# Optimization experiments

Hardware: AMD Instinct MI355X
Metric: run time of the kernel (lower is better)

Reference implementation:

```python
import jax, jax.numpy as jnp
import numpy as np

# SSD prior config (small VGGLite-style)
FEATURE_MAPS = [10, 5, 3, 1]
BOXES_PER_LOC = [4, 4, 4, 4]
IMG = 128      # ssd_config.DATA.SHAPE[0] -> WhereTransformer image_size
OBJ = 64
ZWHAT = 64
HID = 512
B = 4
N_OBJ = sum(f * f for f in FEATURE_MAPS)                       # 135
N_FEAT = sum(b * f * f for f, b in zip(FEATURE_MAPS, BOXES_PER_LOC))  # 540


def reconstruction_indices():
    # Replicates Decoder.reconstruction_indices: map per-location latents to per-box slots.
    idx = []
    last = 0
    for f, bpl in zip(FEATURE_MAPS, BOXES_PER_LOC):
        for i in range(f * f):
            idx.extend([last + i] * bpl)
        last += f * f
    return np.asarray(idx, dtype=np.int32)


def what_decode(z, W1, b1, W2, b2):
    # WhatDecoder: MLP z_what -> 3xOBJxOBJ object glyph in (0,1)
    h = jax.nn.relu(z @ W1 + b1)
    return jax.nn.sigmoid(h @ W2 + b2).reshape(-1, 3, OBJ, OBJ)


def where_stn(imgs, zw):
    # WhereTransformer: paste each object image into its (cx, cy, w, h) box on an IMGxIMG canvas
    # via inverse-affine bilinear sampling with zero padding (STN / grid_sample semantics).
    cx, cy, w, h = zw[:, 0], zw[:, 1], zw[:, 2], zw[:, 3]
    w = jnp.maximum(w, 1e-2)
    h = jnp.maximum(h, 1e-2)
    lin = jnp.linspace(-1.0, 1.0, IMG)
    gy, gx = jnp.meshgrid(lin, lin, indexing='ij')           # (IMG, IMG)
    u = (gx[None] - (2.0 * cx - 1.0)[:, None, None]) / w[:, None, None]
    v = (gy[None] - (2.0 * cy - 1.0)[:, None, None]) / h[:, None, None]
    px = (u + 1.0) * 0.5 * (OBJ - 1)                          # (N, IMG, IMG)
    py = (v + 1.0) * 0.5 * (OBJ - 1)

    def sample_one(img, py, px):  # img: (3, OBJ, OBJ)
        x0 = jnp.floor(px); y0 = jnp.floor(py)
        wx = px - x0; wy = py - y0
        x0i = x0.astype(jnp.int32); y0i = y0.astype(jnp.int32)

        def tap(yi, xi, wgt):
            valid = (yi >= 0) & (yi < OBJ) & (xi >= 0) & (xi < OBJ)
            yc = jnp.clip(yi, 0, OBJ - 1)
            xc = jnp.clip(xi, 0, OBJ - 1)
            return img[:, yc, xc] * (wgt * valid)[None]

        return (tap(y0i, x0i, (1 - wy) * (1 - wx)) + tap(y0i, x0i + 1, (1 - wy) * wx)
                + tap(y0i + 1, x0i, wy * (1 - wx)) + tap(y0i + 1, x0i + 1, wy * wx))

    return jax.vmap(sample_one)(imgs, py, px)                 # (N, 3, IMG, IMG)


def setup_inputs() -> dict:
    key = jax.random.key(0)
    ks = jax.random.split(key, 8)
    return {
        'z_what': jax.random.normal(ks[0], (B, N_OBJ, ZWHAT), jnp.float32),
        'z_where': jax.random.uniform(ks[1], (B, N_FEAT, 4), jnp.float32),
        'z_depth': jax.random.normal(ks[2], (B, N_OBJ, 1), jnp.float32),
        'W1': jax.random.normal(ks[3], (ZWHAT, HID), jnp.float32) * 0.05,
        'b1': jnp.zeros((HID,), jnp.float32),
        'W2': jax.random.normal(ks[4], (HID, 3 * OBJ * OBJ), jnp.float32) * 0.02,
        'b2': jnp.zeros((3 * OBJ * OBJ,), jnp.float32),
        'z_present': jax.random.randint(ks[5], (B, N_FEAT, 1), 0, 2, jnp.int32),
    }


def reference(z_what, z_where, z_depth, W1, b1, W2, b2, z_present):
    idx = jnp.asarray(reconstruction_indices())
    # index_select: replicate per-location latents across boxes-per-location
    zw_full = z_what[:, idx]                                  # (B, N_FEAT, ZWHAT)
    zd_full = z_depth[:, idx]                                 # (B, N_FEAT, 1)
    # sort descending by depth; gather all latents in that order
    order = jnp.argsort(-zd_full[..., 0], axis=1)             # (B, N_FEAT)
    s_what = jnp.take_along_axis(zw_full, order[..., None], axis=1)
    s_where = jnp.take_along_axis(z_where, order[..., None], axis=1)
    s_pres = jnp.take_along_axis(z_present, order[..., None], axis=1)
    # decode + STN warp all objects; absent objects are zeroed (equivalent to the
    dec = what_decode(s_what.reshape(-1, ZWHAT), W1, b1, W2, b2)
    warped = where_stn(dec, s_where.reshape(-1, 4))
    imgs = warped.reshape(B, N_FEAT, 3, IMG, IMG) * s_pres.astype(warped.dtype)[..., None, None]
    # depth compositing: per channel-pixel, take the first nonzero value in sorted order
    nz = imgs != 0
    first = jnp.argmax(nz, axis=1)                            # (B, 3, IMG, IMG)
    out = jnp.take_along_axis(imgs, first[:, None], axis=1)[:, 0] * nz.any(axis=1)
    return out
```

## Files before the change

kernel.cpp:

```cpp
#include <hip/hip_runtime.h>
#include <hip/hip_bf16.h>
#include <math.h>

#define NBOX  540
#define NOBJ  135
#define ZW    64
#define HIDN  512
#define NOUT  12288
#define OBJS  64
#define BATCH 4
#define MROWS 540
#define MPAD  640

#define PRE_SORT   4
#define PRE_GEMM1  MPAD
#define PRE_CVT    ((NOUT / 64) * (HIDN / 64))
#define PRE_BLOCKS (PRE_SORT + PRE_GEMM1 + PRE_CVT)

#define OFF_N      0u
#define OFF_PARAMS 256u
#define OFF_OBJS   34816u
#define OFF_HBF    43520u
#define OFF_W2T    698880u
#define OFF_DEC    13281792u

typedef short  bf16x8 __attribute__((ext_vector_type(8)));
typedef float  f32x4  __attribute__((ext_vector_type(4)));

#define GLOAD_LDS16(gp, lp)                                                    \
  __builtin_amdgcn_global_load_lds(                                            \
      (const __attribute__((address_space(1))) void*)(gp),                     \
      (__attribute__((address_space(3))) void*)(lp), 16, 0, 0)

__device__ __forceinline__ unsigned short f2bf(float x) {
  __hip_bfloat16 h = __float2bfloat16(x);
  return *(unsigned short*)&h;
}

__global__ __launch_bounds__(256) void k_pre(
    const float* __restrict__ z_depth,
    const float* __restrict__ z_where,
    const int*   __restrict__ z_present,
    const float* __restrict__ Z,
    const float* __restrict__ W1,
    const float* __restrict__ b1,
    const float* __restrict__ W2,
    float4* __restrict__ params,
    int*    __restrict__ objs,
    int*    __restrict__ n_present,
    unsigned short* __restrict__ Hbf,
    unsigned short* __restrict__ W2T)
{
  __shared__ unsigned long long keys[256];
  __shared__ int wsums[4], woff[4];
  __shared__ float zs[ZW];
  __shared__ unsigned int T[64 * 36];

  const int bid = blockIdx.x;
  const int t   = threadIdx.x;

  if (bid < PRE_SORT) {
    const int b = bid;
    unsigned long long key = ~0ull;
    if (t < NOBJ) {
      unsigned u = __float_as_uint(z_depth[b * NOBJ + t]);
      u = (u & 0x80000000u) ? ~u : (u | 0x80000000u);
      key = ((unsigned long long)(~u) << 32) | (unsigned)t;
    }
    keys[t] = key;
    __syncthreads();
    for (int k = 2; k <= 256; k <<= 1) {
      for (int j = k >> 1; j > 0; j >>= 1) {
        int ixj = t ^ j;
        if (ixj > t) {
          unsigned long long a = keys[t], c = keys[ixj];
          bool asc = (t & k) == 0;
          if (asc ? (a > c) : (a < c)) { keys[t] = c; keys[ixj] = a; }
        }
        __syncthreads();
      }
    }
    int boxq[3]; int presq[3]; int cnt = 0;
#pragma unroll
    for (int q = 0; q < 3; q++) {
      int e = 3 * t + q;
      presq[q] = 0; boxq[q] = 0;
      if (e < NBOX) {
        int o  = (int)(keys[e >> 2] & 0xFFFFFFFFull);
        int bx = o * 4 + (e & 3);
        boxq[q]  = bx;
        presq[q] = (z_present[b * NBOX + bx] != 0) ? 1 : 0;
        cnt += presq[q];
      }
    }
    int lane = t & 63, wv = t >> 6;
    int incl = cnt;
#pragma unroll
    for (int o = 1; o < 64; o <<= 1) {
      int vprev = __shfl_up(incl, o, 64);
      if (lane >= o) incl += vprev;
    }
    if (lane == 63) wsums[wv] = incl;
    __syncthreads();
    if (t == 0) {
      int a = 0;
#pragma unroll
      for (int i = 0; i < 4; i++) { woff[i] = a; a += wsums[i]; }
      n_present[b] = a;
    }
    __syncthreads();
    int slot = woff[wv] + incl - cnt;
#pragma unroll
    for (int q = 0; q < 3; q++) {
      if (presq[q]) {
        const float* zw = z_where + ((size_t)b * NBOX + boxq[q]) * 4;
        params[b * NBOX + slot] = make_float4(zw[0], zw[1], zw[2], zw[3]);
        objs[b * NBOX + slot]   = boxq[q] >> 2;
        slot++;
      }
    }
  } else if (bid < PRE_SORT + PRE_GEMM1) {
    const int r = bid - PRE_SORT;
    if (r >= MROWS) {
      Hbf[(size_t)r * HIDN + t] = 0;
      Hbf[(size_t)r * HIDN + t + 256] = 0;
      return;
    }
    if (t < ZW) zs[t] = Z[(size_t)r * ZW + t];
    __syncthreads();
    float a0 = b1[t], a1 = b1[t + 256];
#pragma unroll 8
    for (int k = 0; k < ZW; k++) {
      float z = zs[k];
      a0 += z * W1[(size_t)k * HIDN + t];
      a1 += z * W1[(size_t)k * HIDN + t + 256];
    }
    Hbf[(size_t)r * HIDN + t]       = f2bf(fmaxf(a0, 0.f));
    Hbf[(size_t)r * HIDN + t + 256] = f2bf(fmaxf(a1, 0.f));
  } else {
    const int c  = bid - PRE_SORT - PRE_GEMM1;
    const int n0 = (c % (NOUT / 64)) * 64;
    const int k0 = (c / (NOUT / 64)) * 64;
#pragma unroll
    for (int p = 0; p < 2; p++) {
      int kp = p * 16 + (t >> 4);
      int n4 = t & 15;
      int k  = k0 + kp * 2;
      float4 a = *(const float4*)&W2[(size_t)k * NOUT + n0 + n4 * 4];
      float4 b = *(const float4*)&W2[(size_t)(k + 1) * NOUT + n0 + n4 * 4];
      T[(n4*4 + 0) * 36 + kp] = (unsigned)f2bf(a.x) | ((unsigned)f2bf(b.x) << 16);
      T[(n4*4 + 1) * 36 + kp] = (unsigned)f2bf(a.y) | ((unsigned)f2bf(b.y) << 16);
      T[(n4*4 + 2) * 36 + kp] = (unsigned)f2bf(a.z) | ((unsigned)f2bf(b.z) << 16);
      T[(n4*4 + 3) * 36 + kp] = (unsigned)f2bf(a.w) | ((unsigned)f2bf(b.w) << 16);
    }
    __syncthreads();
#pragma unroll
    for (int p = 0; p < 2; p++) {
      int cc = p * 256 + t;
      int n = cc >> 3, ch = cc & 7;
      uint4 v = *(const uint4*)&T[n * 36 + ch * 4];
      *(uint4*)&W2T[(size_t)(n0 + n) * HIDN + k0 + ch * 8] = v;
    }
  }
}

__global__ __launch_bounds__(256) void k_gemm2_mfma(
    const unsigned short* __restrict__ Hbf,
    const unsigned short* __restrict__ W2T,
    const float* __restrict__ b2,
    float* __restrict__ dec)
{
  __shared__ unsigned short As[128 * 32];
  __shared__ unsigned short Bs[128 * 32];
  const int t    = threadIdx.x;
  const int lane = t & 63, wv = t >> 6;
  const int n0 = blockIdx.x * 128;
  const int m0 = blockIdx.y * 128;
  const int wm = (wv & 1) * 64, wn = (wv >> 1) * 64;

  const int r0 = t >> 2;
  const int kc0 = (t & 3) ^ (r0 & 3);
  const int r1 = r0 + 64;
  const int kc1 = (t & 3) ^ (r1 & 3);

  const int fr = lane & 15;
  const int fj = lane >> 4;
  f32x4 acc[4][4] = {};

  for (int k0 = 0; k0 < HIDN; k0 += 32) {
    GLOAD_LDS16(Hbf + (size_t)(m0 + r0) * HIDN + k0 + kc0 * 8, &As[t * 8]);
    GLOAD_LDS16(Hbf + (size_t)(m0 + r1) * HIDN + k0 + kc1 * 8, &As[(t + 256) * 8]);
    GLOAD_LDS16(W2T + (size_t)(n0 + r0) * HIDN + k0 + kc0 * 8, &Bs[t * 8]);
    GLOAD_LDS16(W2T + (size_t)(n0 + r1) * HIDN + k0 + kc1 * 8, &Bs[(t + 256) * 8]);
    __syncthreads();

    bf16x8 av[4], bv[4];
#pragma unroll
    for (int mi = 0; mi < 4; mi++) {
      int row = wm + mi * 16 + fr;
      av[mi] = *(const bf16x8*)&As[(row * 4 + (fj ^ (row & 3))) * 8];
    }
#pragma unroll
    for (int ni = 0; ni < 4; ni++) {
      int row = wn + ni * 16 + fr;
      bv[ni] = *(const bf16x8*)&Bs[(row * 4 + (fj ^ (row & 3))) * 8];
    }
#pragma unroll
    for (int mi = 0; mi < 4; mi++)
#pragma unroll
      for (int ni = 0; ni < 4; ni++)
        acc[mi][ni] = __builtin_amdgcn_mfma_f32_16x16x32_bf16(av[mi], bv[ni], acc[mi][ni], 0, 0, 0);
    __syncthreads();
  }

#pragma unroll
  for (int ni = 0; ni < 4; ni++) {
    int col = n0 + wn + ni * 16 + fr;
    float bb = b2[col];
#pragma unroll
    for (int mi = 0; mi < 4; mi++) {
#pragma unroll
      for (int r = 0; r < 4; r++) {
        int row = m0 + wm + mi * 16 + fj * 4 + r;
        if (row < MROWS) {
          float v = acc[mi][ni][r] + bb;
          dec[(size_t)row * NOUT + col] = 1.0f / (1.0f + __expf(-v));
        }
      }
    }
  }
}

__global__ __launch_bounds__(256) void k_composite(
    const float4* __restrict__ params, const int* __restrict__ objs,
    const int* __restrict__ n_present, const float* __restrict__ dec,
    float* __restrict__ out)
{
#pragma clang fp contract(off)
  __shared__ float4 sp[NBOX];
  __shared__ int sobj[NBOX];
  const int bid  = blockIdx.x;
  const int t    = threadIdx.x;
  const int b    = bid >> 6;
  const int tile = bid & 63;
  const int y = (tile >> 3) * 16 + (t >> 4);
  const int x = (tile & 7) * 16 + (t & 15);
  const int n = n_present[b];
  for (int i = t; i < n; i += 256) {
    sp[i]   = params[b * NBOX + i];
    sobj[i] = objs[b * NBOX + i];
  }
  __syncthreads();

  const double step = 2.0 / 127.0;
  const double gx = (x == 127) ? 1.0 : ((double)x * step + (-1.0));
  const double gy = (y == 127) ? 1.0 : ((double)y * step + (-1.0));

  float o0 = 0.f, o1 = 0.f, o2 = 0.f;
  bool done = false;
  for (int j = 0; j < n; j++) {
    if (__all((int)done)) break;
    if (!done) {
      float4 p = sp[j];
      double w = fmax((double)p.z, 0.01);
      double h = fmax((double)p.w, 0.01);
      double tx = 2.0 * (double)p.x - 1.0;
      double ty = 2.0 * (double)p.y - 1.0;
      double u = (gx - tx) / w;
      double v = (gy - ty) / h;
      double px = (u + 1.0) * 0.5 * 63.0;
      double py = (v + 1.0) * 0.5 * 63.0;
      double fx = floor(px), fy = floor(py);
      double wx = px - fx, wy = py - fy;
      int x0 = (int)fx, y0 = (int)fy;
      int x1 = x0 + 1, y1 = y0 + 1;
      bool vx0 = (x0 >= 0) && (x0 < OBJS);
      bool vx1 = (x1 >= 0) && (x1 < OBJS);
      bool vy0 = (y0 >= 0) && (y0 < OBJS);
      bool vy1 = (y1 >= 0) && (y1 < OBJS);
      double w00 = (1.0 - wy) * (1.0 - wx);
      double w01 = (1.0 - wy) * wx;
      double w10 = wy * (1.0 - wx);
      double w11 = wy * wx;
      bool c00 = vy0 && vx0 && (w00 > 0.0);
      bool c01 = vy0 && vx1 && (w01 > 0.0);
      bool c10 = vy1 && vx0 && (w10 > 0.0);
      bool c11 = vy1 && vx1 && (w11 > 0.0);
      if (c00 | c01 | c10 | c11) {
        const float* g = dec + (size_t)(b * NOBJ + sobj[j]) * NOUT;
        double s0 = 0.0, s1 = 0.0, s2 = 0.0;
        if (c00) { int o = y0*64 + x0; s0 += g[o]*w00; s1 += g[4096+o]*w00; s2 += g[8192+o]*w00; }
        if (c01) { int o = y0*64 + x1; s0 += g[o]*w01; s1 += g[4096+o]*w01; s2 += g[8192+o]*w01; }
        if (c10) { int o = y1*64 + x0; s0 += g[o]*w10; s1 += g[4096+o]*w10; s2 += g[8192+o]*w10; }
        if (c11) { int o = y1*64 + x1; s0 += g[o]*w11; s1 += g[4096+o]*w11; s2 += g[8192+o]*w11; }
        o0 = (float)s0; o1 = (float)s1; o2 = (float)s2;
        done = true;
      }
    }
  }
  const int ob = b * 3 * 16384 + y * 128 + x;
  out[ob]         = o0;
  out[ob + 16384] = o1;
  out[ob + 32768] = o2;
}

extern "C" void kernel_launch(void* const* d_in, const int* in_sizes, int n_in,
                              void* d_out, int out_size, void* d_ws, size_t ws_size,
                              hipStream_t stream) {
  (void)in_sizes; (void)n_in; (void)out_size; (void)ws_size;
  const float* z_what    = (const float*)d_in[0];
  const float* z_where   = (const float*)d_in[1];
  const float* z_depth   = (const float*)d_in[2];
  const float* W1        = (const float*)d_in[3];
  const float* b1        = (const float*)d_in[4];
  const float* W2        = (const float*)d_in[5];
  const float* b2        = (const float*)d_in[6];
  const int*   z_present = (const int*)d_in[7];
  float* out = (float*)d_out;
  char* ws = (char*)d_ws;

  int*            n_present = (int*)(ws + OFF_N);
  float4*         params    = (float4*)(ws + OFF_PARAMS);
  int*            objs      = (int*)(ws + OFF_OBJS);
  unsigned short* Hbf       = (unsigned short*)(ws + OFF_HBF);
  unsigned short* W2T       = (unsigned short*)(ws + OFF_W2T);
  float*          dec       = (float*)(ws + OFF_DEC);

  k_pre<<<dim3(PRE_BLOCKS), dim3(256), 0, stream>>>(
      z_depth, z_where, z_present, z_what, W1, b1, W2,
      params, objs, n_present, Hbf, W2T);
  k_gemm2_mfma<<<dim3(NOUT / 128, MPAD / 128), dim3(256), 0, stream>>>(Hbf, W2T, b2, dec);
  k_composite<<<dim3(256), dim3(256), 0, stream>>>(params, objs, n_present, dec, out);
}
```

Measured before the change: 138.5 us.

## Precompute per-pixel winning objects and decode only visible objects in GEMM

After: 151.2 us. 1.09x slower.

```diff
diff --git a/kernel.cpp b/kernel.cpp
--- a/kernel.cpp
+++ b/kernel.cpp
@@ -9,20 +9,20 @@
 #define NOUT  12288
 #define OBJS  64
 #define BATCH 4
-#define MROWS 540
-#define MPAD  640
-
-#define PRE_SORT   4
-#define PRE_GEMM1  MPAD
-#define PRE_CVT    ((NOUT / 64) * (HIDN / 64))
-#define PRE_BLOCKS (PRE_SORT + PRE_GEMM1 + PRE_CVT)
-
-#define OFF_N      0u
-#define OFF_PARAMS 256u
-#define OFF_OBJS   34816u
-#define OFF_HBF    43520u
-#define OFF_W2T    698880u
-#define OFF_DEC    13281792u
+
+#define ROLE_WIN   256
+#define ROLE_G1    540
+#define ROLE_CVT   ((NOUT / 64) * (HIDN / 64))
+#define PRE_BLOCKS (ROLE_WIN + ROLE_G1 + ROLE_CVT)
+
+#define OFF_NROWS  0u
+#define OFF_USED   256u
+#define OFF_REMAP  2560u
+#define OFF_ROWOBJ 4864u
+#define OFF_PXWIN  7680u
+#define OFF_HBF    269824u
+#define OFF_W2T    925184u
+#define OFF_DEC    13508096u
 
 typedef short  bf16x8 __attribute__((ext_vector_type(8)));
 typedef float  f32x4  __attribute__((ext_vector_type(4)));
@@ -45,22 +45,30 @@
     const float* __restrict__ W1,
     const float* __restrict__ b1,
     const float* __restrict__ W2,
-    float4* __restrict__ params,
-    int*    __restrict__ objs,
-    int*    __restrict__ n_present,
+    int* __restrict__ nrowsp,
+    int* __restrict__ used,
+    int* __restrict__ remap,
+    int* __restrict__ rowobj,
+    int* __restrict__ pxwin,
     unsigned short* __restrict__ Hbf,
     unsigned short* __restrict__ W2T)
 {
   __shared__ unsigned long long keys[256];
-  __shared__ int wsums[4], woff[4];
+  __shared__ float4 sw[NBOX];
+  __shared__ unsigned char spres[NBOX];
   __shared__ float zs[ZW];
   __shared__ unsigned int T[64 * 36];
 
   const int bid = blockIdx.x;
   const int t   = threadIdx.x;
 
-  if (bid < PRE_SORT) {
-    const int b = bid;
+  if (bid < ROLE_WIN) {
+#pragma clang fp contract(off)
+    const int b    = bid >> 6;
+    const int tile = bid & 63;
+    const int y = (tile >> 3) * 16 + (t >> 4);
+    const int x = (tile & 7) * 16 + (t & 15);
+
     unsigned long long key = ~0ull;
     if (t < NOBJ) {
       unsigned u = __float_as_uint(z_depth[b * NOBJ + t]);
@@ -68,6 +76,10 @@
       key = ((unsigned long long)(~u) << 32) | (unsigned)t;
     }
     keys[t] = key;
+    for (int i = t; i < NBOX; i += 256) {
+      sw[i]    = ((const float4*)z_where)[b * NBOX + i];
+      spres[i] = (unsigned char)(z_present[b * NBOX + i] != 0);
+    }
     __syncthreads();
     for (int k = 2; k <= 256; k <<= 1) {
       for (int j = k >> 1; j > 0; j >>= 1) {
@@ -80,52 +92,61 @@
         __syncthreads();
       }
     }
-    int boxq[3]; int presq[3]; int cnt = 0;
-#pragma unroll
-    for (int q = 0; q < 3; q++) {
-      int e = 3 * t + q;
-      presq[q] = 0; boxq[q] = 0;
-      if (e < NBOX) {
-        int o  = (int)(keys[e >> 2] & 0xFFFFFFFFull);
-        int bx = o * 4 + (e & 3);
-        boxq[q]  = bx;
-        presq[q] = (z_present[b * NBOX + bx] != 0) ? 1 : 0;
-        cnt += presq[q];
+
+    const double step = 2.0 / 127.0;
+    const double gx = (x == 127) ? 1.0 : ((double)x * step + (-1.0));
+    const double gy = (y == 127) ? 1.0 : ((double)y * step + (-1.0));
+    const int lane = t & 63;
+
+    bool done = false;
+    int  win  = -1;
+    for (int e = 0; e < NBOX; e++) {
+      if (__all((int)done)) break;
+      const int o  = (int)(keys[e >> 2] & 0xFFFFFFFFull);
+      const int bx = o * 4 + (e & 3);
+      if (!spres[bx]) continue;
+      bool newly = false;
+      if (!done) {
+        float4 p = sw[bx];
+        double w = fmax((double)p.z, 0.01);
+        double h = fmax((double)p.w, 0.01);
+        double tx = 2.0 * (double)p.x - 1.0;
+        double ty = 2.0 * (double)p.y - 1.0;
+        double u = (gx - tx) / w;
+        double v = (gy - ty) / h;
+        double px = (u + 1.0) * 0.5 * 63.0;
+        double py = (v + 1.0) * 0.5 * 63.0;
+        double fx = floor(px), fy = floor(py);
+        double wx = px - fx, wy = py - fy;
+        int x0 = (int)fx, y0 = (int)fy;
+        int x1 = x0 + 1, y1 = y0 + 1;
+        bool vx0 = (x0 >= 0) && (x0 < OBJS);
+        bool vx1 = (x1 >= 0) && (x1 < OBJS);
+        bool vy0 = (y0 >= 0) && (y0 < OBJS);
+        bool vy1 = (y1 >= 0) && (y1 < OBJS);
+        double w00 = (1.0 - wy) * (1.0 - wx);
+        double w01 = (1.0 - wy) * wx;
+        double w10 = wy * (1.0 - wx);
+        double w11 = wy * wx;
+        bool c00 = vy0 && vx0 && (w00 > 0.0);
+        bool c01 = vy0 && vx1 && (w01 > 0.0);
+        bool c10 = vy1 && vx0 && (w10 > 0.0);
+        bool c11 = vy1 && vx1 && (w11 > 0.0);
+        if (c00 | c01 | c10 | c11) { win = bx; done = true; newly = true; }
       }
-    }
-    int lane = t & 63, wv = t >> 6;
-    int incl = cnt;
-#pragma unroll
-    for (int o = 1; o < 64; o <<= 1) {
-      int vprev = __shfl_up(incl, o, 64);
-      if (lane >= o) incl += vprev;
-    }
-    if (lane == 63) wsums[wv] = incl;
-    __syncthreads();
-    if (t == 0) {
-      int a = 0;
-#pragma unroll
-      for (int i = 0; i < 4; i++) { woff[i] = a; a += wsums[i]; }
-      n_present[b] = a;
-    }
-    __syncthreads();
-    int slot = woff[wv] + incl - cnt;
-#pragma unroll
-    for (int q = 0; q < 3; q++) {
-      if (presq[q]) {
-        const float* zw = z_where + ((size_t)b * NBOX + boxq[q]) * 4;
-        params[b * NBOX + slot] = make_float4(zw[0], zw[1], zw[2], zw[3]);
-        objs[b * NBOX + slot]   = boxq[q] >> 2;
-        slot++;
+      unsigned long long nm = __ballot((int)newly);
+      if (nm != 0ull && lane == (int)__builtin_ctzll(nm)) {
+        int oi = b * NOBJ + o;
+        if (atomicCAS(&used[oi], 0, 1) == 0) {
+          int rr = atomicAdd(nrowsp, 1);
+          rowobj[rr] = oi;
+          remap[oi]  = rr;
+        }
       }
     }
-  } else if (bid < PRE_SORT + PRE_GEMM1) {
-    const int r = bid - PRE_SORT;
-    if (r >= MROWS) {
-      Hbf[(size_t)r * HIDN + t] = 0;
-      Hbf[(size_t)r * HIDN + t + 256] = 0;
-      return;
-    }
+    pxwin[b * 16384 + y * 128 + x] = win;
+  } else if (bid < ROLE_WIN + ROLE_G1) {
+    const int r = bid - ROLE_WIN;
     if (t < ZW) zs[t] = Z[(size_t)r * ZW + t];
     __syncthreads();
     float a0 = b1[t], a1 = b1[t + 256];
@@ -138,7 +159,7 @@
     Hbf[(size_t)r * HIDN + t]       = f2bf(fmaxf(a0, 0.f));
     Hbf[(size_t)r * HIDN + t + 256] = f2bf(fmaxf(a1, 0.f));
   } else {
-    const int c  = bid - PRE_SORT - PRE_GEMM1;
+    const int c  = bid - ROLE_WIN - ROLE_G1;
     const int n0 = (c % (NOUT / 64)) * 64;
     const int k0 = (c / (NOUT / 64)) * 64;
 #pragma unroll
@@ -168,42 +189,62 @@
     const unsigned short* __restrict__ Hbf,
     const unsigned short* __restrict__ W2T,
     const float* __restrict__ b2,
+    const int* __restrict__ nrowsp,
+    const int* __restrict__ rowobj,
     float* __restrict__ dec)
 {
-  __shared__ unsigned short As[128 * 32];
-  __shared__ unsigned short Bs[128 * 32];
+  __shared__ unsigned short As[2][128 * 32];
+  __shared__ unsigned short Bs[2][128 * 32];
+  const int nr = *nrowsp;
+  int bid = (int)blockIdx.x;
+  bid = (bid & 7) * 60 + (bid >> 3);
+  const int m0 = (bid / 96) * 128;
+  if (m0 >= nr) return;
+  const int n0 = (bid % 96) * 128;
+
   const int t    = threadIdx.x;
   const int lane = t & 63, wv = t >> 6;
-  const int n0 = blockIdx.x * 128;
-  const int m0 = blockIdx.y * 128;
   const int wm = (wv & 1) * 64, wn = (wv >> 1) * 64;
 
-  const int r0 = t >> 2;
+  const int r0  = t >> 2;
   const int kc0 = (t & 3) ^ (r0 & 3);
-  const int r1 = r0 + 64;
+  const int r1  = r0 + 64;
   const int kc1 = (t & 3) ^ (r1 & 3);
+
+  const int ga0 = (m0 + r0 < nr) ? rowobj[m0 + r0] : 0;
+  const int ga1 = (m0 + r1 < nr) ? rowobj[m0 + r1] : 0;
+  const unsigned short* a0p = Hbf + (size_t)ga0 * HIDN + kc0 * 8;
+  const unsigned short* a1p = Hbf + (size_t)ga1 * HIDN + kc1 * 8;
+  const unsigned short* b0p = W2T + (size_t)(n0 + r0) * HIDN + kc0 * 8;
+  const unsigned short* b1p = W2T + (size_t)(n0 + r1) * HIDN + kc1 * 8;
 
   const int fr = lane & 15;
   const int fj = lane >> 4;
   f32x4 acc[4][4] = {};
 
-  for (int k0 = 0; k0 < HIDN; k0 += 32) {
-    GLOAD_LDS16(Hbf + (size_t)(m0 + r0) * HIDN + k0 + kc0 * 8, &As[t * 8]);
-    GLOAD_LDS16(Hbf + (size_t)(m0 + r1) * HIDN + k0 + kc1 * 8, &As[(t + 256) * 8]);
-    GLOAD_LDS16(W2T + (size_t)(n0 + r0) * HIDN + k0 + kc0 * 8, &Bs[t * 8]);
-    GLOAD_LDS16(W2T + (size_t)(n0 + r1) * HIDN + k0 + kc1 * 8, &Bs[(t + 256) * 8]);
-    __syncthreads();
-
+#define STAGE(buf, koff)                                                       \
+  do {                                                                         \
+    GLOAD_LDS16(a0p + (koff), &As[buf][t * 8]);                                \
+    GLOAD_LDS16(a1p + (koff), &As[buf][(t + 256) * 8]);                        \
+    GLOAD_LDS16(b0p + (koff), &Bs[buf][t * 8]);                                \
+    GLOAD_LDS16(b1p + (koff), &Bs[buf][(t + 256) * 8]);                        \
+  } while (0)
+
+  STAGE(0, 0);
+  __syncthreads();
+  int cur = 0;
+  for (int kt = 0; kt < HIDN / 32; ++kt) {
+    if (kt < HIDN / 32 - 1) STAGE(cur ^ 1, (kt + 1) * 32);
     bf16x8 av[4], bv[4];
 #pragma unroll
     for (int mi = 0; mi < 4; mi++) {
       int row = wm + mi * 16 + fr;
-      av[mi] = *(const bf16x8*)&As[(row * 4 + (fj ^ (row & 3))) * 8];
+      av[mi] = *(const bf16x8*)&As[cur][(row * 4 + (fj ^ (row & 3))) * 8];
     }
 #pragma unroll
     for (int ni = 0; ni < 4; ni++) {
       int row = wn + ni * 16 + fr;
-      bv[ni] = *(const bf16x8*)&Bs[(row * 4 + (fj ^ (row & 3))) * 8];
+      bv[ni] = *(const bf16x8*)&Bs[cur][(row * 4 + (fj ^ (row & 3))) * 8];
     }
 #pragma unroll
     for (int mi = 0; mi < 4; mi++)
@@ -211,7 +252,9 @@
       for (int ni = 0; ni < 4; ni++)
         acc[mi][ni] = __builtin_amdgcn_mfma_f32_16x16x32_bf16(av[mi], bv[ni], acc[mi][ni], 0, 0, 0);
     __syncthreads();
+    cur ^= 1;
   }
+#undef STAGE
 
 #pragma unroll
   for (int ni = 0; ni < 4; ni++) {
@@ -222,81 +265,65 @@
 #pragma unroll
       for (int r = 0; r < 4; r++) {
         int row = m0 + wm + mi * 16 + fj * 4 + r;
-        if (row < MROWS) {
-          float v = acc[mi][ni][r] + bb;
-          dec[(size_t)row * NOUT + col] = 1.0f / (1.0f + __expf(-v));
-        }
+        float v = acc[mi][ni][r] + bb;
+        dec[(size_t)row * NOUT + col] = 1.0f / (1.0f + __expf(-v));
       }
     }
   }
 }
 
 __global__ __launch_bounds__(256) void k_composite(
-    const float4* __restrict__ params, const int* __restrict__ objs,
-    const int* __restrict__ n_present, const float* __restrict__ dec,
+    const int* __restrict__ pxwin, const int* __restrict__ remap,
+    const float* __restrict__ z_where, const float* __restrict__ dec,
     float* __restrict__ out)
 {
 #pragma clang fp contract(off)
-  __shared__ float4 sp[NBOX];
-  __shared__ int sobj[NBOX];
   const int bid  = blockIdx.x;
   const int t    = threadIdx.x;
   const int b    = bid >> 6;
   const int tile = bid & 63;
   const int y = (tile >> 3) * 16 + (t >> 4);
   const int x = (tile & 7) * 16 + (t & 15);
-  const int n = n_present[b];
-  for (int i = t; i < n; i += 256) {
-    sp[i]   = params[b * NBOX + i];
-    sobj[i] = objs[b * NBOX + i];
-  }
-  __syncthreads();
-
-  const double step = 2.0 / 127.0;
-  const double gx = (x == 127) ? 1.0 : ((double)x * step + (-1.0));
-  const double gy = (y == 127) ? 1.0 : ((double)y * step + (-1.0));
-
+
+  const int win = pxwin[b * 16384 + y * 128 + x];
   float o0 = 0.f, o1 = 0.f, o2 = 0.f;
-  bool done = false;
-  for (int j = 0; j < n; j++) {
-    if (__all((int)done)) break;
-    if (!done) {
-      float4 p = sp[j];
-      double w = fmax((double)p.z, 0.01);
-      double h = fmax((double)p.w, 0.01);
-      double tx = 2.0 * (double)p.x - 1.0;
-      double ty = 2.0 * (double)p.y - 1.0;
-      double u = (gx - tx) / w;
-      double v = (gy - ty) / h;
-      double px = (u + 1.0) * 0.5 * 63.0;
-      double py = (v + 1.0) * 0.5 * 63.0;
-      double fx = floor(px), fy = floor(py);
-      double wx = px - fx, wy = py - fy;
-      int x0 = (int)fx, y0 = (int)fy;
-      int x1 = x0 + 1, y1 = y0 + 1;
-      bool vx0 = (x0 >= 0) && (x0 < OBJS);
-      bool vx1 = (x1 >= 0) && (x1 < OBJS);
-      bool vy0 = (y0 >= 0) && (y0 < OBJS);
-      bool vy1 = (y1 >= 0) && (y1 < OBJS);
-      double w00 = (1.0 - wy) * (1.0 - wx);
-      double w01 = (1.0 - wy) * wx;
-      double w10 = wy * (1.0 - wx);
-      double w11 = wy * wx;
-      bool c00 = vy0 && vx0 && (w00 > 0.0);
-      bool c01 = vy0 && vx1 && (w01 > 0.0);
-      bool c10 = vy1 && vx0 && (w10 > 0.0);
-      bool c11 = vy1 && vx1 && (w11 > 0.0);
-      if (c00 | c01 | c10 | c11) {
-        const float* g = dec + (size_t)(b * NOBJ + sobj[j]) * NOUT;
-        double s0 = 0.0, s1 = 0.0, s2 = 0.0;
-        if (c00) { int o = y0*64 + x0; s0 += g[o]*w00; s1 += g[4096+o]*w00; s2 += g[8192+o]*w00; }
-        if (c01) { int o = y0*64 + x1; s0 += g[o]*w01; s1 += g[4096+o]*w01; s2 += g[8192+o]*w01; }
-        if (c10) { int o = y1*64 + x0; s0 += g[o]*w10; s1 += g[4096+o]*w10; s2 += g[8192+o]*w10; }
-        if (c11) { int o = y1*64 + x1; s0 += g[o]*w11; s1 += g[4096+o]*w11; s2 += g[8192+o]*w11; }
-        o0 = (float)s0; o1 = (float)s1; o2 = (float)s2;
-        done = true;
-      }
-    }
+  if (win >= 0) {
+    const float4 p = ((const float4*)z_where)[b * NBOX + win];
+    const double step = 2.0 / 127.0;
+    const double gx = (x == 127) ? 1.0 : ((double)x * step + (-1.0));
+    const double gy = (y == 127) ? 1.0 : ((double)y * step + (-1.0));
+    double w = fmax((double)p.z, 0.01);
+    double h = fmax((double)p.w, 0.01);
+    double tx = 2.0 * (double)p.x - 1.0;
+    double ty = 2.0 * (double)p.y - 1.0;
+    double u = (gx - tx) / w;
+    double v = (gy - ty) / h;
+    double px = (u + 1.0) * 0.5 * 63.0;
+    double py = (v + 1.0) * 0.5 * 63.0;
+    double fx = floor(px), fy = floor(py);
+    double wx = px - fx, wy = py - fy;
+    int x0 = (int)fx, y0 = (int)fy;
+    int x1 = x0 + 1, y1 = y0 + 1;
+    bool vx0 = (x0 >= 0) && (x0 < OBJS);
+    bool vx1 = (x1 >= 0) && (x1 < OBJS);
+    bool vy0 = (y0 >= 0) && (y0 < OBJS);
+    bool vy1 = (y1 >= 0) && (y1 < OBJS);
+    double w00 = (1.0 - wy) * (1.0 - wx);
+    double w01 = (1.0 - wy) * wx;
+    double w10 = wy * (1.0 - wx);
+    double w11 = wy * wx;
+    bool c00 = vy0 && vx0 && (w00 > 0.0);
+    bool c01 = vy0 && vx1 && (w01 > 0.0);
+    bool c10 = vy1 && vx0 && (w10 > 0.0);
+    bool c11 = vy1 && vx1 && (w11 > 0.0);
+    const int row = remap[b * NOBJ + (win >> 2)];
+    const float* g = dec + (size_t)row * NOUT;
+    double s0 = 0.0, s1 = 0.0, s2 = 0.0;
+    if (c00) { int o = y0*64 + x0; s0 += g[o]*w00; s1 += g[4096+o]*w00; s2 += g[8192+o]*w00; }
+    if (c01) { int o = y0*64 + x1; s0 += g[o]*w01; s1 += g[4096+o]*w01; s2 += g[8192+o]*w01; }
+    if (c10) { int o = y1*64 + x0; s0 += g[o]*w10; s1 += g[4096+o]*w10; s2 += g[8192+o]*w10; }
+    if (c11) { int o = y1*64 + x1; s0 += g[o]*w11; s1 += g[4096+o]*w11; s2 += g[8192+o]*w11; }
+    o0 = (float)s0; o1 = (float)s1; o2 = (float)s2;
   }
   const int ob = b * 3 * 16384 + y * 128 + x;
   out[ob]         = o0;
@@ -319,16 +346,21 @@
   float* out = (float*)d_out;
   char* ws = (char*)d_ws;
 
-  int*            n_present = (int*)(ws + OFF_N);
-  float4*         params    = (float4*)(ws + OFF_PARAMS);
-  int*            objs      = (int*)(ws + OFF_OBJS);
-  unsigned short* Hbf       = (unsigned short*)(ws + OFF_HBF);
-  unsigned short* W2T       = (unsigned short*)(ws + OFF_W2T);
-  float*          dec       = (float*)(ws + OFF_DEC);
+  int*            nrowsp = (int*)(ws + OFF_NROWS);
+  int*            used   = (int*)(ws + OFF_USED);
+  int*            remap  = (int*)(ws + OFF_REMAP);
+  int*            rowobj = (int*)(ws + OFF_ROWOBJ);
+  int*            pxwin  = (int*)(ws + OFF_PXWIN);
+  unsigned short* Hbf    = (unsigned short*)(ws + OFF_HBF);
+  unsigned short* W2T    = (unsigned short*)(ws + OFF_W2T);
+  float*          dec    = (float*)(ws + OFF_DEC);
+
+  hipMemsetAsync(ws + OFF_NROWS, 0, 2560, stream);
 
   k_pre<<<dim3(PRE_BLOCKS), dim3(256), 0, stream>>>(
       z_depth, z_where, z_present, z_what, W1, b1, W2,
-      params, objs, n_present, Hbf, W2T);
-  k_gemm2_mfma<<<dim3(NOUT / 128, MPAD / 128), dim3(256), 0, stream>>>(Hbf, W2T, b2, dec);
-  k_composite<<<dim3(256), dim3(256), 0, stream>>>(params, objs, n_present, dec, out);
-}
+      nrowsp, used, remap, rowobj, pxwin, Hbf, W2T);
+  k_gemm2_mfma<<<dim3((NOUT / 128) * 5), dim3(256), 0, stream>>>(
+      Hbf, W2T, b2, nrowsp, rowobj, dec);
+  k_composite<<<dim3(256), dim3(256), 0, stream>>>(pxwin, remap, z_where, dec, out);
+}
```
